# Kernel tuning notes

Measured on AMD Instinct MI355X. Metric: run time of the kernel, lower is better.

## Reference

```python
import jax, jax.numpy as jnp
import numpy as np

EMBED_DIM = 2048
NUM_HEADS = 16
HEAD_DIM = EMBED_DIM // NUM_HEADS
ROPE_BASE = 10000.0


def setup_inputs() -> dict:
    key = jax.random.key(0)
    ks = jax.random.split(key, 5)
    s = 1.0 / np.sqrt(EMBED_DIM)
    return {
        "x": jax.random.normal(ks[0], (2, 2048, EMBED_DIM), dtype=jnp.float32),
        "Wq": jax.random.normal(ks[1], (EMBED_DIM, EMBED_DIM), dtype=jnp.float32) * s,
        "Wk": jax.random.normal(ks[2], (EMBED_DIM, EMBED_DIM), dtype=jnp.float32) * s,
        "Wv": jax.random.normal(ks[3], (EMBED_DIM, EMBED_DIM), dtype=jnp.float32) * s,
        "Wo": jax.random.normal(ks[4], (EMBED_DIM, EMBED_DIM), dtype=jnp.float32) * s,
    }


def _rope(x):
    # x: [b, h, s, d]; standard rotate-half RoPE
    b, h, s, d = x.shape
    inv_freq = 1.0 / (ROPE_BASE ** (jnp.arange(0, d, 2, dtype=jnp.float32) / d))
    ang = jnp.arange(s, dtype=jnp.float32)[:, None] * inv_freq[None, :]  # [s, d/2]
    cos = jnp.concatenate([jnp.cos(ang), jnp.cos(ang)], axis=-1)  # [s, d]
    sin = jnp.concatenate([jnp.sin(ang), jnp.sin(ang)], axis=-1)
    x1, x2 = x[..., : d // 2], x[..., d // 2 :]
    rot = jnp.concatenate([-x2, x1], axis=-1)
    return x * cos + rot * sin


def reference(x, Wq, Wk, Wv, Wo):
    b, s, e = x.shape
    h, d = NUM_HEADS, HEAD_DIM
    # projections (torch Linear: x @ W.T); W here stored so that y = x @ W
    q = (x @ Wq).reshape(b, s, h, d).transpose(0, 2, 1, 3)
    k = (x @ Wk).reshape(b, s, h, d).transpose(0, 2, 1, 3)
    v = (x @ Wv).reshape(b, s, h, d).transpose(0, 2, 1, 3)
    q = _rope(q)
    k = _rope(k)
    att = jnp.einsum("bhqd,bhkd->bhqk", q, k) / jnp.sqrt(jnp.float32(d))
    causal = jnp.tril(jnp.ones((s, s), dtype=bool))
    att = jnp.where(causal, att, -jnp.inf)
    att = jax.nn.softmax(att, axis=-1)
    out = jnp.einsum("bhqk,bhkd->bhqd", att, v)
    out = out.transpose(0, 2, 1, 3).reshape(b, s, e)
    return out @ Wo
```

## Files before the change

### kernel.cpp

```cpp
#include <hip/hip_runtime.h>
#include <stdint.h>

#define EDIM 2048
#define HH 16
#define DD 128
#define SS 2048
#define BB 2

typedef __attribute__((ext_vector_type(8))) __bf16 bf16x8;
typedef __attribute__((ext_vector_type(8))) unsigned short ushort8;
typedef __attribute__((ext_vector_type(4))) unsigned short ushort4v;
typedef __attribute__((ext_vector_type(4))) float f32x4;

__device__ __forceinline__ unsigned short f2b(float f) {
    union { float f; unsigned int u; } v; v.f = f;
    unsigned int u = v.u;
    unsigned int r = (u + 0x7fffu + ((u >> 16) & 1u)) >> 16;
    return (unsigned short)r;
}
__device__ __forceinline__ float b2f(unsigned short h) {
    union { unsigned int u; float f; } v; v.u = ((unsigned int)h) << 16;
    return v.f;
}
__device__ __forceinline__ bf16x8 lds8(const unsigned short* p) {
    return __builtin_bit_cast(bf16x8, *(const ushort8*)p);
}
__device__ __forceinline__ void gl_lds16(const unsigned short* g, unsigned short* l) {
    __builtin_amdgcn_global_load_lds(
        (const __attribute__((address_space(1))) void*)(const void*)g,
        (__attribute__((address_space(3))) void*)(void*)l, 16, 0, 0);
}
__device__ __forceinline__ float fexp2(float x) {
    float r;
    asm volatile("v_exp_f32 %0, %1\n\ts_nop 1" : "=v"(r) : "v"(x));
    return r;
}


__global__ __launch_bounds__(256) void k_cvt_x(const float4* __restrict__ x,
                                               ushort4v* __restrict__ xb) {
    size_t i = (size_t)blockIdx.x * 256 + threadIdx.x;
    float4 v = x[i];
    ushort4v o;
    o.x = f2b(v.x); o.y = f2b(v.y); o.z = f2b(v.z); o.w = f2b(v.w);
    xb[i] = o;
}

__global__ __launch_bounds__(256) void k_trans(const float* __restrict__ W0,
                                               const float* __restrict__ W1,
                                               const float* __restrict__ W2,
                                               const float* __restrict__ W3,
                                               unsigned short* __restrict__ Wt) {
    const float* W = (blockIdx.z == 0) ? W0 : (blockIdx.z == 1) ? W1
                     : (blockIdx.z == 2) ? W2 : W3;
    unsigned short* out = Wt + (size_t)blockIdx.z * EDIM * EDIM;
    __shared__ float t[64][65];
    int r0 = blockIdx.y * 64, c0 = blockIdx.x * 64;
#pragma unroll
    for (int i = 0; i < 16; ++i) {
        int e = threadIdx.x + i * 256; int r = e >> 6, c = e & 63;
        t[r][c] = W[(size_t)(r0 + r) * EDIM + c0 + c];
    }
    __syncthreads();
#pragma unroll
    for (int i = 0; i < 16; ++i) {
        int e = threadIdx.x + i * 256; int r = e >> 6, c = e & 63;
        out[(size_t)(c0 + r) * EDIM + r0 + c] = f2b(t[c][r]);
    }
}


__device__ __forceinline__ void gemm_core(const unsigned short* __restrict__ A,
                                          const unsigned short* __restrict__ Bt,
                                          int K, size_t m0, size_t n0,
                                          unsigned short* As, unsigned short* Bs,
                                          f32x4 acc[4][4], int wave, int lane) {
    const int wm = wave >> 1, wn = wave & 1;
    const int lg = lane >> 4, lr = lane & 15;
    for (int kt = 0; kt < K; kt += 32) {
#pragma unroll
        for (int j = 0; j < 2; ++j) {
            const int cb = j * 256 + wave * 64;
            const int c  = cb + lane;
            gl_lds16(A  + (m0 + (size_t)(c >> 2)) * K + kt + (c & 3) * 8, As + cb * 8);
            gl_lds16(Bt + (n0 + (size_t)(c >> 2)) * K + kt + (c & 3) * 8, Bs + cb * 8);
        }
        __syncthreads();
        bf16x8 af[4], bg[4];
#pragma unroll
        for (int i = 0; i < 4; ++i) {
            af[i] = lds8(As + (wm * 64 + i * 16 + lr) * 32 + lg * 8);
            bg[i] = lds8(Bs + (wn * 64 + i * 16 + lr) * 32 + lg * 8);
        }
#pragma unroll
        for (int i = 0; i < 4; ++i)
#pragma unroll
            for (int j = 0; j < 4; ++j)
                acc[i][j] = __builtin_amdgcn_mfma_f32_16x16x32_bf16(af[i], bg[j], acc[i][j], 0, 0, 0);
        __syncthreads();
    }
}

__global__ __launch_bounds__(256) void k_gemm_qkv(const unsigned short* __restrict__ xb,
                                                  const unsigned short* __restrict__ Wt,
                                                  unsigned short* __restrict__ Qd,
                                                  unsigned short* __restrict__ Kd,
                                                  unsigned short* __restrict__ Vtd) {
    __shared__ alignas(16) unsigned short As[128 * 32];
    __shared__ alignas(16) unsigned short Bs[128 * 32];
    const int tid = threadIdx.x, wave = tid >> 6, lane = tid & 63;
    const int wsel = blockIdx.y >> 4;
    const size_t m0 = (size_t)blockIdx.x * 128;
    const size_t n0 = (size_t)(blockIdx.y & 15) * 128;
    const unsigned short* Bw = Wt + (size_t)wsel * EDIM * EDIM;
    f32x4 acc[4][4] = {};
    gemm_core(xb, Bw, EDIM, m0, n0, As, Bs, acc, wave, lane);
    const int wm = wave >> 1, wn = wave & 1, lg = lane >> 4, lr = lane & 15;
    if (wsel < 2) {
        unsigned short* dst = wsel ? Kd : Qd;
#pragma unroll
        for (int i = 0; i < 4; ++i)
#pragma unroll
            for (int j = 0; j < 4; ++j)
#pragma unroll
                for (int r = 0; r < 4; ++r) {
                    int row = (int)m0 + wm * 64 + i * 16 + lg * 4 + r;
                    int e   = (int)n0 + wn * 64 + j * 16 + lr;
                    int b = row >> 11, s = row & (SS - 1);
                    int h = e >> 7,  d = e & (DD - 1);
                    dst[(((size_t)(b * HH + h)) * SS + s) * DD + d] = f2b(acc[i][j][r]);
                }
    } else {
#pragma unroll
        for (int i = 0; i < 4; ++i)
#pragma unroll
            for (int j = 0; j < 4; ++j) {
                int row0 = (int)m0 + wm * 64 + i * 16 + lg * 4;
                int e    = (int)n0 + wn * 64 + j * 16 + lr;
                int b = row0 >> 11, s0 = row0 & (SS - 1);
                int h = e >> 7, d = e & (DD - 1);
                ushort4v pk;
                pk.x = f2b(acc[i][j][0]); pk.y = f2b(acc[i][j][1]);
                pk.z = f2b(acc[i][j][2]); pk.w = f2b(acc[i][j][3]);
                *(ushort4v*)(Vtd + (((size_t)(b * HH + h)) * DD + d) * SS + s0) = pk;
            }
    }
}

__global__ __launch_bounds__(256) void k_gemm_out(const unsigned short* __restrict__ Ob,
                                                  const unsigned short* __restrict__ Wto,
                                                  float* __restrict__ y) {
    __shared__ alignas(16) unsigned short As[128 * 32];
    __shared__ alignas(16) unsigned short Bs[128 * 32];
    const int tid = threadIdx.x, wave = tid >> 6, lane = tid & 63;
    const size_t m0 = (size_t)blockIdx.x * 128;
    const size_t n0 = (size_t)blockIdx.y * 128;
    f32x4 acc[4][4] = {};
    gemm_core(Ob, Wto, EDIM, m0, n0, As, Bs, acc, wave, lane);
    const int wm = wave >> 1, wn = wave & 1, lg = lane >> 4, lr = lane & 15;
#pragma unroll
    for (int i = 0; i < 4; ++i)
#pragma unroll
        for (int j = 0; j < 4; ++j)
#pragma unroll
            for (int r = 0; r < 4; ++r) {
                size_t row = m0 + wm * 64 + i * 16 + lg * 4 + r;
                size_t col = n0 + wn * 64 + j * 16 + lr;
                y[row * EDIM + col] = acc[i][j][r];
            }
}


__global__ __launch_bounds__(256) void k_rope(unsigned short* __restrict__ Q,
                                              unsigned short* __restrict__ K) {
    int idx = blockIdx.x * 256 + threadIdx.x;
    int i  = idx & 63;
    int s  = (idx >> 6) & (SS - 1);
    int bh = idx >> 17;
    size_t base = ((size_t)bh * SS + s) * DD;
    float inv = __expf(-0.14391156608f * (float)i);
    float ang = (float)s * inv;
    float sn, cs; sincosf(ang, &sn, &cs);
    const float qs = 0.08838834764831845f * 1.44269504088896340736f;
    float q1 = b2f(Q[base + i]), q2 = b2f(Q[base + 64 + i]);
    float k1 = b2f(K[base + i]), k2 = b2f(K[base + 64 + i]);
    Q[base + i]      = f2b((q1 * cs - q2 * sn) * qs);
    Q[base + 64 + i] = f2b((q2 * cs + q1 * sn) * qs);
    K[base + i]      = f2b(k1 * cs - k2 * sn);
    K[base + 64 + i] = f2b(k2 * cs + k1 * sn);
}


__device__ __forceinline__ void attn_tile(const unsigned short* Ks, const unsigned short* Vs,
                                          unsigned short* Ps, const bf16x8 qf[4],
                                          f32x4 o[9], bool maskdiag,
                                          int wave, int lg, int lr) {
    f32x4 sa[4] = {};
    __builtin_amdgcn_s_setprio(1);
#pragma unroll
    for (int nf = 0; nf < 4; ++nf)
#pragma unroll
        for (int kk = 0; kk < 4; ++kk) {
            bf16x8 kb = lds8(Ks + (nf * 16 + lr) * 136 + kk * 32 + lg * 8);
            sa[nf] = __builtin_amdgcn_mfma_f32_16x16x32_bf16(qf[kk], kb, sa[nf], 0, 0, 0);
        }
    __builtin_amdgcn_s_setprio(0);
    if (maskdiag) {
#pragma unroll
        for (int nf = 0; nf < 4; ++nf)
#pragma unroll
            for (int r = 0; r < 4; ++r) {
                int col = nf * 16 + lr, rw = wave * 16 + lg * 4 + r;
                if (col > rw) sa[nf][r] = -__builtin_inff();
            }
    }
#pragma unroll
    for (int nf = 0; nf < 4; ++nf)
#pragma unroll
        for (int r = 0; r < 4; ++r) {
            float p = fexp2(sa[nf][r]);
            unsigned int u = __builtin_bit_cast(unsigned int, p);
            Ps[(wave * 16 + lg * 4 + r) * 72 + nf * 16 + lr] =
                (unsigned short)((u + 0x8000u) >> 16);
        }
    bf16x8 pa0 = lds8(Ps + (wave * 16 + lr) * 72 + lg * 8);
    bf16x8 pa1 = lds8(Ps + (wave * 16 + lr) * 72 + 32 + lg * 8);
    __builtin_amdgcn_s_setprio(1);
#pragma unroll
    for (int nf = 0; nf < 9; ++nf) {
        bf16x8 v0 = lds8(Vs + (nf * 16 + lr) * 72 + lg * 8);
        bf16x8 v1 = lds8(Vs + (nf * 16 + lr) * 72 + 32 + lg * 8);
        o[nf] = __builtin_amdgcn_mfma_f32_16x16x32_bf16(pa0, v0, o[nf], 0, 0, 0);
        o[nf] = __builtin_amdgcn_mfma_f32_16x16x32_bf16(pa1, v1, o[nf], 0, 0, 0);
    }
    __builtin_amdgcn_s_setprio(0);
}

__global__ __launch_bounds__(256) void k_attn(const unsigned short* __restrict__ Q,
                                              const unsigned short* __restrict__ Kg,
                                              const unsigned short* __restrict__ Vt,
                                              unsigned short* __restrict__ Ob) {
    __shared__ alignas(16) unsigned short Ks[64 * 136];
    __shared__ alignas(16) unsigned short Vs[144 * 72];
    __shared__ alignas(16) unsigned short Ps[64 * 72];
    const int tid = threadIdx.x, wave = tid >> 6, lane = tid & 63;
    const int lg = lane >> 4, lr = lane & 15;
    const int bh = blockIdx.y;
    const int tp = blockIdx.x;
    const int qa0 = tp * 64, qb0 = (31 - tp) * 64;
    const int nta = tp + 1, ntb = 32 - tp;
    const size_t qkb = (size_t)bh * SS * DD;
    const size_t vbb = (size_t)bh * DD * SS;

    {
        ushort4v one4; one4.x = 0x3F80; one4.y = 0x3F80; one4.z = 0x3F80; one4.w = 0x3F80;
        *(ushort4v*)(Vs + (128 + (tid >> 4)) * 72 + (tid & 15) * 4) = one4;
    }

    bf16x8 qfA[4], qfB[4];
    {
        const unsigned short* qpA = Q + qkb + (size_t)(qa0 + wave * 16 + lr) * DD + lg * 8;
        const unsigned short* qpB = Q + qkb + (size_t)(qb0 + wave * 16 + lr) * DD + lg * 8;
#pragma unroll
        for (int kk = 0; kk < 4; ++kk) {
            qfA[kk] = __builtin_bit_cast(bf16x8, *(const ushort8*)(qpA + kk * 32));
            qfB[kk] = __builtin_bit_cast(bf16x8, *(const ushort8*)(qpB + kk * 32));
        }
    }
    f32x4 oA[9] = {}, oB[9] = {};

    ushort8 kr[4], vr[4];
#pragma unroll
    for (int i = 0; i < 4; ++i) {
        int c = tid + i * 256;
        kr[i] = *(const ushort8*)(Kg + qkb + (size_t)(c >> 4) * DD + (c & 15) * 8);
        vr[i] = *(const ushort8*)(Vt + vbb + (size_t)(c >> 3) * SS + (c & 7) * 8);
    }

    for (int t = 0; t < ntb; ++t) {
        __syncthreads();
#pragma unroll
        for (int i = 0; i < 4; ++i) {
            int c = tid + i * 256;
            *(ushort8*)(Ks + (c >> 4) * 136 + (c & 15) * 8) = kr[i];
            *(ushort8*)(Vs + (c >> 3) * 72 + (c & 7) * 8) = vr[i];
        }
        __syncthreads();
        if (t + 1 < ntb) {
            int kv0 = (t + 1) * 64;
#pragma unroll
            for (int i = 0; i < 4; ++i) {
                int c = tid + i * 256;
                kr[i] = *(const ushort8*)(Kg + qkb + (size_t)(kv0 + (c >> 4)) * DD + (c & 15) * 8);
                vr[i] = *(const ushort8*)(Vt + vbb + (size_t)(c >> 3) * SS + kv0 + (c & 7) * 8);
            }
        }
        attn_tile(Ks, Vs, Ps, qfB, oB, t == ntb - 1, wave, lg, lr);
        if (t < nta)
            attn_tile(Ks, Vs, Ps, qfA, oA, t == nta - 1, wave, lg, lr);
    }

    const int b = bh >> 4, h = bh & 15;
#pragma unroll
    for (int nf = 0; nf < 8; ++nf)
#pragma unroll
        for (int r = 0; r < 4; ++r) {
            int sA = qa0 + wave * 16 + lg * 4 + r;
            int sB = qb0 + wave * 16 + lg * 4 + r;
            int e = h * DD + nf * 16 + lr;
            Ob[((size_t)b * SS + sA) * EDIM + e] = f2b(oA[nf][r] / oA[8][r]);
            Ob[((size_t)b * SS + sB) * EDIM + e] = f2b(oB[nf][r] / oB[8][r]);
        }
}


extern "C" void kernel_launch(void* const* d_in, const int* in_sizes, int n_in,
                              void* d_out, int out_size, void* d_ws, size_t ws_size,
                              hipStream_t stream) {
    const float* x  = (const float*)d_in[0];
    const float* Wq = (const float*)d_in[1];
    const float* Wk = (const float*)d_in[2];
    const float* Wv = (const float*)d_in[3];
    const float* Wo = (const float*)d_in[4];
    float* y = (float*)d_out;
    char* ws = (char*)d_ws;
    unsigned short* xb  = (unsigned short*)(ws);
    unsigned short* Wt  = (unsigned short*)(ws + (size_t)16777216);
    unsigned short* Qd  = (unsigned short*)(ws + (size_t)50331648);
    unsigned short* Kd  = (unsigned short*)(ws + (size_t)67108864);
    unsigned short* Vtd = (unsigned short*)(ws + (size_t)83886080);
    unsigned short* Ob  = (unsigned short*)(ws + (size_t)100663296);

    hipLaunchKernelGGL(k_cvt_x, dim3(8192), dim3(256), 0, stream, (const float4*)x, (ushort4v*)xb);
    hipLaunchKernelGGL(k_trans, dim3(32, 32, 4), dim3(256), 0, stream, Wq, Wk, Wv, Wo, Wt);
    hipLaunchKernelGGL(k_gemm_qkv, dim3(32, 48), dim3(256), 0, stream, xb, Wt, Qd, Kd, Vtd);
    hipLaunchKernelGGL(k_rope, dim3(16384), dim3(256), 0, stream, Qd, Kd);
    hipLaunchKernelGGL(k_attn, dim3(16, 32), dim3(256), 0, stream, Qd, Kd, Vtd, Ob);
    hipLaunchKernelGGL(k_gemm_out, dim3(32, 16), dim3(256), 0, stream,
                       Ob, Wt + (size_t)3 * EDIM * EDIM, y);
}
```

Before: 419.3 us.

## Rewrite QKV GEMM with 256x256 tiles, double-buffered swizzled LDS, and XCD-aware block mapping

Replaces the QKV projection GEMM with a 512-thread kernel that computes 256x256 output tiles with K-step 64. It double-buffers A and B in LDS using an XOR swizzle and interleaves the global-to-LDS prefetches with MFMA phases under explicit waitcnt and barriers. Block indices are remapped so that consecutive blocks land on the same XCD, and the output GEMM gets the same remapping. The aim is more data reuse per tile, hiding load latency, and better L2 locality, at the cost of higher register and LDS use and fewer blocks in flight.

```diff
diff --git a/kernel.cpp b/kernel.cpp
--- a/kernel.cpp
+++ b/kernel.cpp
@@ -6,11 +6,14 @@
 #define DD 128
 #define SS 2048
 #define BB 2
+#define NT2 32
 
 typedef __attribute__((ext_vector_type(8))) __bf16 bf16x8;
 typedef __attribute__((ext_vector_type(8))) unsigned short ushort8;
 typedef __attribute__((ext_vector_type(4))) unsigned short ushort4v;
 typedef __attribute__((ext_vector_type(4))) float f32x4;
+
+#define MFMA16 __builtin_amdgcn_mfma_f32_16x16x32_bf16
 
 __device__ __forceinline__ unsigned short f2b(float f) {
     union { float f; unsigned int u; } v; v.f = f;
@@ -34,6 +37,10 @@
     float r;
     asm volatile("v_exp_f32 %0, %1\n\ts_nop 1" : "=v"(r) : "v"(x));
     return r;
+}
+__device__ __forceinline__ void barrier_np() {
+    __builtin_amdgcn_s_barrier();
+    __builtin_amdgcn_sched_barrier(0);
 }
 
 
@@ -70,6 +77,147 @@
 }
 
 
+__device__ __forceinline__ void stage16(const unsigned short* __restrict__ G,
+                                        unsigned short* L, int wave, int lane, int s) {
+    int q  = (s * 8 + wave) * 1024 + lane * 16;
+    int qp = q ^ (((q >> 7) & 7) << 4);
+    int row = qp >> 7, col = (qp & 127) >> 1;
+    gl_lds16(G + (size_t)row * EDIM + col, L + (s * 8 + wave) * 512);
+}
+__device__ __forceinline__ bf16x8 frag_read(const unsigned short* Lhalf,
+                                            int rowl, int kk, int lg) {
+    int b = rowl * 128 + kk * 64 + lg * 16;
+    b ^= ((b >> 7) & 7) << 4;
+    return lds8(Lhalf + (b >> 1));
+}
+
+#define QKV_PHASE(MF0) do {                                                    \
+    bf16x8 a00 = frag_read(Ah, (MF0) * 16 + lr, 0, lg);                        \
+    bf16x8 a01 = frag_read(Ah, (MF0) * 16 + lr, 1, lg);                        \
+    bf16x8 a10 = frag_read(Ah, (MF0) * 16 + 16 + lr, 0, lg);                   \
+    bf16x8 a11 = frag_read(Ah, (MF0) * 16 + 16 + lr, 1, lg);                   \
+    __builtin_amdgcn_s_setprio(1);                                             \
+    _Pragma("unroll")                                                          \
+    for (int nf = 0; nf < 4; ++nf) {                                           \
+        acc[(MF0)][nf]     = MFMA16(a00, bfr[nf][0], acc[(MF0)][nf], 0, 0, 0); \
+        acc[(MF0)][nf]     = MFMA16(a01, bfr[nf][1], acc[(MF0)][nf], 0, 0, 0); \
+        acc[(MF0) + 1][nf] = MFMA16(a10, bfr[nf][0], acc[(MF0) + 1][nf], 0, 0, 0); \
+        acc[(MF0) + 1][nf] = MFMA16(a11, bfr[nf][1], acc[(MF0) + 1][nf], 0, 0, 0); \
+    }                                                                          \
+    __builtin_amdgcn_s_setprio(0);                                             \
+} while (0)
+
+__global__ __launch_bounds__(512) void k_gemm_qkv2(const unsigned short* __restrict__ xb,
+                                                   const unsigned short* __restrict__ Wt,
+                                                   unsigned short* __restrict__ Qd,
+                                                   unsigned short* __restrict__ Kd,
+                                                   unsigned short* __restrict__ Vtd) {
+    __shared__ alignas(16) unsigned short As[2][2][8192];
+    __shared__ alignas(16) unsigned short Bs[2][2][8192];
+    const int tid = threadIdx.x, wave = tid >> 6, lane = tid & 63;
+    const int lr = lane & 15, lg = lane >> 4;
+    const int wm = wave >> 2, wn = wave & 3;
+    const int nb   = (blockIdx.x & 7) * 48 + (blockIdx.x >> 3);
+    const int wsel = nb >> 7, rr = nb & 127;
+    const size_t m0 = (size_t)(rr & 15) * 256;
+    const size_t n0 = (size_t)(rr >> 4) * 256;
+    const unsigned short* A  = xb;
+    const unsigned short* Bw = Wt + (size_t)wsel * EDIM * EDIM;
+
+    f32x4 acc[8][4] = {};
+
+#pragma unroll
+    for (int h = 0; h < 2; ++h)
+#pragma unroll
+        for (int s = 0; s < 2; ++s)
+            stage16(Bw + (n0 + h * 128) * EDIM, Bs[0][h], wave, lane, s);
+#pragma unroll
+    for (int h = 0; h < 2; ++h)
+#pragma unroll
+        for (int s = 0; s < 2; ++s)
+            stage16(A + (m0 + h * 128) * EDIM, As[0][h], wave, lane, s);
+#pragma unroll
+    for (int h = 0; h < 2; ++h)
+#pragma unroll
+        for (int s = 0; s < 2; ++s)
+            stage16(Bw + (n0 + h * 128) * EDIM + 64, Bs[1][h], wave, lane, s);
+    asm volatile("s_waitcnt vmcnt(4)" ::: "memory");
+    __builtin_amdgcn_sched_barrier(0);
+    barrier_np();
+
+    for (int u = 0; u < NT2; ++u) {
+        const int cur = u & 1;
+        const unsigned short* Ah = As[cur][wm];
+        bf16x8 bfr[4][2];
+#pragma unroll
+        for (int nf = 0; nf < 4; ++nf) {
+            int nl = wn * 64 + nf * 16 + lr;
+            const unsigned short* Bh = Bs[cur][nl >> 7];
+#pragma unroll
+            for (int kk = 0; kk < 2; ++kk)
+                bfr[nf][kk] = frag_read(Bh, nl & 127, kk, lg);
+        }
+        QKV_PHASE(0);
+        barrier_np();
+        if (u + 1 < NT2) {
+#pragma unroll
+            for (int h = 0; h < 2; ++h)
+#pragma unroll
+                for (int s = 0; s < 2; ++s)
+                    stage16(A + (m0 + h * 128) * EDIM + (u + 1) * 64,
+                            As[(u + 1) & 1][h], wave, lane, s);
+        }
+        QKV_PHASE(2);
+        barrier_np();
+        if (u + 2 < NT2) {
+#pragma unroll
+            for (int h = 0; h < 2; ++h)
+#pragma unroll
+                for (int s = 0; s < 2; ++s)
+                    stage16(Bw + (n0 + h * 128) * EDIM + (u + 2) * 64,
+                            Bs[cur][h], wave, lane, s);
+        }
+        QKV_PHASE(4);
+        barrier_np();
+        QKV_PHASE(6);
+        if (u + 2 < NT2) asm volatile("s_waitcnt vmcnt(4)" ::: "memory");
+        else             asm volatile("s_waitcnt vmcnt(0)" ::: "memory");
+        __builtin_amdgcn_sched_barrier(0);
+        barrier_np();
+    }
+
+    if (wsel < 2) {
+        unsigned short* dst = wsel ? Kd : Qd;
+#pragma unroll
+        for (int mf = 0; mf < 8; ++mf)
+#pragma unroll
+            for (int nf = 0; nf < 4; ++nf)
+#pragma unroll
+                for (int r = 0; r < 4; ++r) {
+                    int row = (int)m0 + wm * 128 + mf * 16 + lg * 4 + r;
+                    int e   = (int)n0 + wn * 64 + nf * 16 + lr;
+                    int b = row >> 11, s = row & (SS - 1);
+                    int h = e >> 7,  d = e & (DD - 1);
+                    dst[(((size_t)(b * HH + h)) * SS + s) * DD + d] = f2b(acc[mf][nf][r]);
+                }
+    } else {
+#pragma unroll
+        for (int mf = 0; mf < 8; ++mf)
+#pragma unroll
+            for (int nf = 0; nf < 4; ++nf) {
+                int row0 = (int)m0 + wm * 128 + mf * 16 + lg * 4;
+                int e    = (int)n0 + wn * 64 + nf * 16 + lr;
+                int b = row0 >> 11, s0 = row0 & (SS - 1);
+                int h = e >> 7, d = e & (DD - 1);
+                ushort4v pk;
+                pk.x = f2b(acc[mf][nf][0]); pk.y = f2b(acc[mf][nf][1]);
+                pk.z = f2b(acc[mf][nf][2]); pk.w = f2b(acc[mf][nf][3]);
+                *(ushort4v*)(Vtd + (((size_t)(b * HH + h)) * DD + d) * SS + s0) = pk;
+            }
+    }
+}
+
+
 __device__ __forceinline__ void gemm_core(const unsigned short* __restrict__ A,
                                           const unsigned short* __restrict__ Bt,
                                           int K, size_t m0, size_t n0,
@@ -96,54 +244,8 @@
         for (int i = 0; i < 4; ++i)
 #pragma unroll
             for (int j = 0; j < 4; ++j)
-                acc[i][j] = __builtin_amdgcn_mfma_f32_16x16x32_bf16(af[i], bg[j], acc[i][j], 0, 0, 0);
+                acc[i][j] = MFMA16(af[i], bg[j], acc[i][j], 0, 0, 0);
         __syncthreads();
-    }
-}
-
-__global__ __launch_bounds__(256) void k_gemm_qkv(const unsigned short* __restrict__ xb,
-                                                  const unsigned short* __restrict__ Wt,
-                                                  unsigned short* __restrict__ Qd,
-                                                  unsigned short* __restrict__ Kd,
-                                                  unsigned short* __restrict__ Vtd) {
-    __shared__ alignas(16) unsigned short As[128 * 32];
-    __shared__ alignas(16) unsigned short Bs[128 * 32];
-    const int tid = threadIdx.x, wave = tid >> 6, lane = tid & 63;
-    const int wsel = blockIdx.y >> 4;
-    const size_t m0 = (size_t)blockIdx.x * 128;
-    const size_t n0 = (size_t)(blockIdx.y & 15) * 128;
-    const unsigned short* Bw = Wt + (size_t)wsel * EDIM * EDIM;
-    f32x4 acc[4][4] = {};
-    gemm_core(xb, Bw, EDIM, m0, n0, As, Bs, acc, wave, lane);
-    const int wm = wave >> 1, wn = wave & 1, lg = lane >> 4, lr = lane & 15;
-    if (wsel < 2) {
-        unsigned short* dst = wsel ? Kd : Qd;
-#pragma unroll
-        for (int i = 0; i < 4; ++i)
-#pragma unroll
-            for (int j = 0; j < 4; ++j)
-#pragma unroll
-                for (int r = 0; r < 4; ++r) {
-                    int row = (int)m0 + wm * 64 + i * 16 + lg * 4 + r;
-                    int e   = (int)n0 + wn * 64 + j * 16 + lr;
-                    int b = row >> 11, s = row & (SS - 1);
-                    int h = e >> 7,  d = e & (DD - 1);
-                    dst[(((size_t)(b * HH + h)) * SS + s) * DD + d] = f2b(acc[i][j][r]);
-                }
-    } else {
-#pragma unroll
-        for (int i = 0; i < 4; ++i)
-#pragma unroll
-            for (int j = 0; j < 4; ++j) {
-                int row0 = (int)m0 + wm * 64 + i * 16 + lg * 4;
-                int e    = (int)n0 + wn * 64 + j * 16 + lr;
-                int b = row0 >> 11, s0 = row0 & (SS - 1);
-                int h = e >> 7, d = e & (DD - 1);
-                ushort4v pk;
-                pk.x = f2b(acc[i][j][0]); pk.y = f2b(acc[i][j][1]);
-                pk.z = f2b(acc[i][j][2]); pk.w = f2b(acc[i][j][3]);
-                *(ushort4v*)(Vtd + (((size_t)(b * HH + h)) * DD + d) * SS + s0) = pk;
-            }
     }
 }
 
@@ -153,8 +255,9 @@
     __shared__ alignas(16) unsigned short As[128 * 32];
     __shared__ alignas(16) unsigned short Bs[128 * 32];
     const int tid = threadIdx.x, wave = tid >> 6, lane = tid & 63;
-    const size_t m0 = (size_t)blockIdx.x * 128;
-    const size_t n0 = (size_t)blockIdx.y * 128;
+    const int nb = (blockIdx.x & 7) * 64 + (blockIdx.x >> 3);
+    const size_t m0 = (size_t)(nb & 31) * 128;
+    const size_t n0 = (size_t)(nb >> 5) * 128;
     f32x4 acc[4][4] = {};
     gemm_core(Ob, Wto, EDIM, m0, n0, As, Bs, acc, wave, lane);
     const int wm = wave >> 1, wn = wave & 1, lg = lane >> 4, lr = lane & 15;
@@ -202,7 +305,7 @@
 #pragma unroll
         for (int kk = 0; kk < 4; ++kk) {
             bf16x8 kb = lds8(Ks + (nf * 16 + lr) * 136 + kk * 32 + lg * 8);
-            sa[nf] = __builtin_amdgcn_mfma_f32_16x16x32_bf16(qf[kk], kb, sa[nf], 0, 0, 0);
+            sa[nf] = MFMA16(qf[kk], kb, sa[nf], 0, 0, 0);
         }
     __builtin_amdgcn_s_setprio(0);
     if (maskdiag) {
@@ -230,8 +333,8 @@
     for (int nf = 0; nf < 9; ++nf) {
         bf16x8 v0 = lds8(Vs + (nf * 16 + lr) * 72 + lg * 8);
         bf16x8 v1 = lds8(Vs + (nf * 16 + lr) * 72 + 32 + lg * 8);
-        o[nf] = __builtin_amdgcn_mfma_f32_16x16x32_bf16(pa0, v0, o[nf], 0, 0, 0);
-        o[nf] = __builtin_amdgcn_mfma_f32_16x16x32_bf16(pa1, v1, o[nf], 0, 0, 0);
+        o[nf] = MFMA16(pa0, v0, o[nf], 0, 0, 0);
+        o[nf] = MFMA16(pa1, v1, o[nf], 0, 0, 0);
     }
     __builtin_amdgcn_s_setprio(0);
 }
@@ -251,12 +354,10 @@
     const int nta = tp + 1, ntb = 32 - tp;
     const size_t qkb = (size_t)bh * SS * DD;
     const size_t vbb = (size_t)bh * DD * SS;
-
     {
         ushort4v one4; one4.x = 0x3F80; one4.y = 0x3F80; one4.z = 0x3F80; one4.w = 0x3F80;
         *(ushort4v*)(Vs + (128 + (tid >> 4)) * 72 + (tid & 15) * 4) = one4;
     }
-
     bf16x8 qfA[4], qfB[4];
     {
         const unsigned short* qpA = Q + qkb + (size_t)(qa0 + wave * 16 + lr) * DD + lg * 8;
@@ -268,7 +369,6 @@
         }
     }
     f32x4 oA[9] = {}, oB[9] = {};
-
     ushort8 kr[4], vr[4];
 #pragma unroll
     for (int i = 0; i < 4; ++i) {
@@ -276,7 +376,6 @@
         kr[i] = *(const ushort8*)(Kg + qkb + (size_t)(c >> 4) * DD + (c & 15) * 8);
         vr[i] = *(const ushort8*)(Vt + vbb + (size_t)(c >> 3) * SS + (c & 7) * 8);
     }
-
     for (int t = 0; t < ntb; ++t) {
         __syncthreads();
 #pragma unroll
@@ -299,7 +398,6 @@
         if (t < nta)
             attn_tile(Ks, Vs, Ps, qfA, oA, t == nta - 1, wave, lg, lr);
     }
-
     const int b = bh >> 4, h = bh & 15;
 #pragma unroll
     for (int nf = 0; nf < 8; ++nf)
@@ -333,9 +431,9 @@
 
     hipLaunchKernelGGL(k_cvt_x, dim3(8192), dim3(256), 0, stream, (const float4*)x, (ushort4v*)xb);
     hipLaunchKernelGGL(k_trans, dim3(32, 32, 4), dim3(256), 0, stream, Wq, Wk, Wv, Wo, Wt);
-    hipLaunchKernelGGL(k_gemm_qkv, dim3(32, 48), dim3(256), 0, stream, xb, Wt, Qd, Kd, Vtd);
+    hipLaunchKernelGGL(k_gemm_qkv2, dim3(384), dim3(512), 0, stream, xb, Wt, Qd, Kd, Vtd);
     hipLaunchKernelGGL(k_rope, dim3(16384), dim3(256), 0, stream, Qd, Kd);
     hipLaunchKernelGGL(k_attn, dim3(16, 32), dim3(256), 0, stream, Qd, Kd, Vtd, Ob);
-    hipLaunchKernelGGL(k_gemm_out, dim3(32, 16), dim3(256), 0, stream,
+    hipLaunchKernelGGL(k_gemm_out, dim3(512), dim3(256), 0, stream,
                        Ob, Wt + (size_t)3 * EDIM * EDIM, y);
 }
```

After: 421.7 us. No clear change (+0.6%).
